# Optimization experiments

Measured on AMD Instinct MI355X. Metric: run time of the kernel, lower is better.

The kernel has to match this reference:

```python
import jax, jax.numpy as jnp
import numpy as np

N_GENE, N_DRUG = 20000, 3000
D_GENE, D_DRUG = 1024, 512
H = [256, 128]
E_GG, E_DD, E_DT = 600000, 120000, 150000
P_DROP = 0.2


def _dropout(x, key):
    # F.dropout(p=0.2, training=True) with a fixed key for determinism
    keep = jax.random.bernoulli(key, 1.0 - P_DROP, x.shape)
    return jnp.where(keep, x / (1.0 - P_DROP), 0.0).astype(x.dtype)


def _gcn_norm(x, W, b, edge_index, n):
    src, dst = edge_index[0], edge_index[1]
    loops = jnp.arange(n, dtype=src.dtype)
    src = jnp.concatenate([src, loops])
    dst = jnp.concatenate([dst, loops])
    deg = jax.ops.segment_sum(jnp.ones(src.shape, x.dtype), dst, num_segments=n)
    dinv = jax.lax.rsqrt(deg)  # deg >= 1 thanks to self loops
    xw = x @ W  # [n_src, out]
    msg = xw[src] * (dinv[src] * dinv[dst])[:, None]  # [E+n, out]
    return jax.ops.segment_sum(msg, dst, num_segments=n) + b


def _gcn_plain(x, W, b, edge_index, n_dst):
    # PyG GCNConv(add_self_loops=False, normalize=False): A X W + b (bipartite scatter)
    xw = x @ W
    return jax.ops.segment_sum(xw[edge_index[0]], edge_index[1], num_segments=n_dst) + b


def _l2norm(x):
    # F.normalize(dim=1, p=2), eps=1e-12
    n = jnp.linalg.norm(x, axis=1, keepdims=True)
    return x / jnp.maximum(n, 1e-12)


def setup_inputs() -> dict:
    key = jax.random.key(0)
    ks = jax.random.split(key, 32)
    inp = {}
    inp["gene_feat"] = jax.random.normal(ks[0], (N_GENE, D_GENE), jnp.float32)
    inp["drug_feat"] = jax.random.normal(ks[1], (N_DRUG, D_DRUG), jnp.float32)
    inp["ei_gg"] = jax.random.randint(ks[2], (2, E_GG), 0, N_GENE)
    inp["ei_dd"] = jax.random.randint(ks[3], (2, E_DD), 0, N_DRUG)
    # drug_target: messages from drug (src row) to gene (dst row)
    inp["ei_dt"] = jnp.stack([jax.random.randint(ks[4], (E_DT,), 0, N_DRUG),
                               jax.random.randint(ks[5], (E_DT,), 0, N_GENE)])
    # target_drug: messages from gene (src row) to drug (dst row)
    inp["ei_td"] = jnp.stack([jax.random.randint(ks[6], (E_DT,), 0, N_GENE),
                               jax.random.randint(ks[7], (E_DT,), 0, N_DRUG)])
    dims_in = {"gg": D_GENE, "dd": D_DRUG, "dt": D_DRUG, "td": D_GENE}
    i = 8
    for l, h in enumerate(H):
        for et in ["gg", "dd", "dt", "td"]:
            din = dims_in[et] if l == 0 else H[l - 1]
            s = float(1.0 / np.sqrt(din))
            inp[f"W{l}_{et}"] = jax.random.uniform(ks[i], (din, h), jnp.float32, -s, s)
            i += 1
            inp[f"b{l}_{et}"] = jnp.zeros((h,), jnp.float32)
    return inp


def reference(gene_feat, drug_feat, ei_gg, ei_dd, ei_dt, ei_td,
              W0_gg, b0_gg, W0_dd, b0_dd, W0_dt, b0_dt, W0_td, b0_td,
              W1_gg, b1_gg, W1_dd, b1_dd, W1_dt, b1_dt, W1_td, b1_td):
    dk = jax.random.split(jax.random.key(42), 8)
    layers = [
        ((W0_gg, b0_gg), (W0_dd, b0_dd), (W0_dt, b0_dt), (W0_td, b0_td)),
        ((W1_gg, b1_gg), (W1_dd, b1_dd), (W1_dt, b1_dt), (W1_td, b1_td)),
    ]
    xg, xd = gene_feat, drug_feat
    k = 0
    for (Wgg, bgg), (Wdd, bdd), (Wdt, bdt), (Wtd, btd) in layers:
        gg = jax.nn.relu(_gcn_norm(_dropout(xg, dk[k + 0]), Wgg, bgg, ei_gg, N_GENE))
        dd = jax.nn.relu(_gcn_norm(_dropout(xd, dk[k + 1]), Wdd, bdd, ei_dd, N_DRUG))
        dt = jax.nn.relu(_gcn_plain(_dropout(xd, dk[k + 2]), Wdt, bdt, ei_dt, N_GENE))
        td = jax.nn.relu(_gcn_plain(_dropout(xg, dk[k + 3]), Wtd, btd, ei_td, N_DRUG))
        # per-edge-type L2 normalize, then sum contributions per node type
        xg = _l2norm(gg) + _l2norm(dt)
        xd = _l2norm(dd) + _l2norm(td)
        k += 4
    # concat node-type outputs: genes first, drugs second -> [N_GENE+N_DRUG, H[-1]]
    return jnp.concatenate([xg, xd], axis=0)
```

## Files before the change

kernel.cpp:

```cpp
#include <hip/hip_runtime.h>
#include <stdint.h>

#define N_GENE 20000
#define N_DRUG 3000
#define D_GENE 1024
#define D_DRUG 512
#define H0 256
#define H1 128
#define E_GG 600000
#define E_DD 120000
#define E_DT 150000

typedef __attribute__((ext_vector_type(8))) short bf16x8;
typedef __attribute__((ext_vector_type(4))) float f32x4;

__host__ __device__ inline uint32_t rotl32(uint32_t x, int d) {
#ifdef __HIP_DEVICE_COMPILE__
    return __builtin_amdgcn_alignbit(x, x, 32 - d);
#else
    return (x << d) | (x >> (32 - d));
#endif
}

__host__ __device__ inline void tf2x32(uint32_t k0, uint32_t k1, uint32_t x0, uint32_t x1,
                                       uint32_t& o0, uint32_t& o1) {
    uint32_t ks2 = k0 ^ k1 ^ 0x1BD11BDAu;
    x0 += k0; x1 += k1;
#define TFR(r) { x0 += x1; x1 = rotl32(x1, r); x1 ^= x0; }
    TFR(13) TFR(15) TFR(26) TFR(6)
    x0 += k1; x1 += ks2 + 1u;
    TFR(17) TFR(29) TFR(16) TFR(24)
    x0 += ks2; x1 += k0 + 2u;
    TFR(13) TFR(15) TFR(26) TFR(6)
    x0 += k0; x1 += k1 + 3u;
    TFR(17) TFR(29) TFR(16) TFR(24)
    x0 += k1; x1 += ks2 + 4u;
    TFR(13) TFR(15) TFR(26) TFR(6)
    x0 += ks2; x1 += k0 + 5u;
#undef TFR
    o0 = x0; o1 = x1;
}

__device__ inline float bf_lo(uint32_t u) { return __uint_as_float(u << 16); }
__device__ inline float bf_hi(uint32_t u) { return __uint_as_float(u & 0xFFFF0000u); }

__device__ inline uint32_t drnd(float x, unsigned idx, uint32_t k0, uint32_t k1) {
    uint32_t a, b;
    tf2x32(k0, k1, 0u, idx, a, b);
    uint32_t bits = a ^ b;
    uint32_t u = __float_as_uint(x);
    uint32_t r = ((u + 0x7FFFu + ((u >> 16) & 1u)) >> 16) & 0xFFFFu;
    return ((bits >> 9) < 6710887u) ? r : 0u;
}

__device__ inline short f2bf(float f) {
    uint32_t u = __float_as_uint(f);
    uint32_t r = (u + 0x7FFFu + ((u >> 16) & 1u)) >> 16;
    return (short)r;
}

#define CUM_E0 600000u
#define CUM_E1 720000u
#define CUM_E2 870000u
#define CUM_E3 1020000u

struct Cast4P {
    unsigned c0, c1, c2, c3;
    uint32_t k0a, k1a, k0b, k1b, k0c, k1c, k0d, k1d;
};
__global__ __launch_bounds__(256) void cast4_kernel(const float* __restrict__ Xg,
                                                    const float* __restrict__ Xd,
                                                    short* __restrict__ Am, Cast4P P) {
    unsigned j = (blockIdx.x * 256u + threadIdx.x) * 8u;
    if (j >= P.c3) return;
    unsigned base; uint32_t k0, k1; const float* X;
    if (j >= P.c2)      { base = P.c2; k0 = P.k0d; k1 = P.k1d; X = Xd; }
    else if (j >= P.c1) { base = P.c1; k0 = P.k0c; k1 = P.k1c; X = Xd; }
    else if (j >= P.c0) { base = P.c0; k0 = P.k0b; k1 = P.k1b; X = Xg; }
    else                { base = 0u;   k0 = P.k0a; k1 = P.k1a; X = Xg; }
    unsigned local = j - base;
    float4 xa = *(const float4*)(X + local);
    float4 xb = *(const float4*)(X + local + 4);
    uint32_t w0 = drnd(xa.x, local + 0u, k0, k1) | (drnd(xa.y, local + 1u, k0, k1) << 16);
    uint32_t w1 = drnd(xa.z, local + 2u, k0, k1) | (drnd(xa.w, local + 3u, k0, k1) << 16);
    uint32_t w2 = drnd(xb.x, local + 4u, k0, k1) | (drnd(xb.y, local + 5u, k0, k1) << 16);
    uint32_t w3 = drnd(xb.z, local + 6u, k0, k1) | (drnd(xb.w, local + 7u, k0, k1) << 16);
    *(uint4*)(Am + j) = make_uint4(w0, w1, w2, w3);
}

__global__ void count4_kernel(const int* __restrict__ gg, const int* __restrict__ dd,
                              const int* __restrict__ dt, const int* __restrict__ td,
                              int* __restrict__ cnt) {
    unsigned e = blockIdx.x * 256u + threadIdx.x;
    if (e >= CUM_E3) return;
    const int* dsts; unsigned base, noff;
    if (e >= CUM_E2)      { dsts = td + E_DT; base = CUM_E2; noff = 43000; }
    else if (e >= CUM_E1) { dsts = dt + E_DT; base = CUM_E1; noff = 23000; }
    else if (e >= CUM_E0) { dsts = dd + E_DD; base = CUM_E0; noff = 20000; }
    else                  { dsts = gg + E_GG; base = 0;      noff = 0; }
    atomicAdd(&cnt[noff + dsts[e - base]], 1);
}

__global__ __launch_bounds__(1024) void scan_p1(const int* __restrict__ cnt,
                                                int* __restrict__ tmp, int* __restrict__ bsum) {
    __shared__ int buf[1024];
    int tid = threadIdx.x;
    int i = blockIdx.x * 1024 + tid;
    int v = (i < 46000) ? cnt[i] : 0;
    buf[tid] = v;
    __syncthreads();
    for (int off = 1; off < 1024; off <<= 1) {
        int t = (tid >= off) ? buf[tid - off] : 0;
        __syncthreads();
        buf[tid] += t;
        __syncthreads();
    }
    if (i < 46000) tmp[i] = buf[tid];
    if (tid == 1023) bsum[blockIdx.x] = buf[1023];
}

__global__ void scan_p2(int* __restrict__ bsum) {
    int lane = threadIdx.x;
    int v = (lane < 45) ? bsum[lane] : 0;
    int orig = v;
    for (int off = 1; off < 64; off <<= 1) {
        int t = __shfl_up(v, off, 64);
        if (lane >= off) v += t;
    }
    if (lane < 45) bsum[lane] = v - orig;
}

__global__ __launch_bounds__(1024) void scan_p3(const int* __restrict__ cnt,
                                                const int* __restrict__ tmp,
                                                const int* __restrict__ bsum,
                                                int* __restrict__ rpall, int* __restrict__ pos,
                                                float* __restrict__ dinv_g,
                                                float* __restrict__ dinv_d) {
    int i = blockIdx.x * 1024 + threadIdx.x;
    if (i < 46000) {
        int g = tmp[i] - cnt[i] + bsum[blockIdx.x];
        rpall[i] = g;
        pos[i] = g;
        if (i < 20000) dinv_g[i] = 1.0f / sqrtf((float)cnt[i] + 1.0f);
        else if (i < 23000) dinv_d[i - 20000] = 1.0f / sqrtf((float)cnt[i] + 1.0f);
    }
    if (i == 0) rpall[46000] = (int)CUM_E3;
}

struct CastT4P {
    unsigned c0, c1, c2, c3;
    int lgK0, lgK1, lgK2, lgK3;
    int N;
};
__device__ inline void castT_body(unsigned idx, const float* W0, const float* W1,
                                  const float* W2, const float* W3,
                                  short* __restrict__ Wt, const CastT4P& P) {
    if (idx >= P.c3) return;
    unsigned base; const float* W; int lgK;
    if (idx >= P.c2)      { base = P.c2; W = W3; lgK = P.lgK3; }
    else if (idx >= P.c1) { base = P.c1; W = W2; lgK = P.lgK2; }
    else if (idx >= P.c0) { base = P.c0; W = W1; lgK = P.lgK1; }
    else                  { base = 0u;   W = W0; lgK = P.lgK0; }
    unsigned local = idx - base;
    unsigned n = local >> lgK, k = local & ((1u << lgK) - 1u);
    Wt[idx] = f2bf(W[(size_t)k * P.N + n]);
}

__global__ __launch_bounds__(256) void fillcastT_kernel(
    const int* __restrict__ gg, const int* __restrict__ dd,
    const int* __restrict__ dt, const int* __restrict__ td,
    int* __restrict__ pos, int* __restrict__ col,
    const float* __restrict__ W0, const float* __restrict__ W1,
    const float* __restrict__ W2, const float* __restrict__ W3,
    short* __restrict__ Wt, CastT4P P, int fillBlocks) {
    int bx = blockIdx.x;
    if (bx < fillBlocks) {
        unsigned e = (unsigned)bx * 256u + threadIdx.x;
        if (e >= CUM_E3) return;
        const int* ei; unsigned base, noff; int E;
        if (e >= CUM_E2)      { ei = td; base = CUM_E2; noff = 43000; E = E_DT; }
        else if (e >= CUM_E1) { ei = dt; base = CUM_E1; noff = 23000; E = E_DT; }
        else if (e >= CUM_E0) { ei = dd; base = CUM_E0; noff = 20000; E = E_DD; }
        else                  { ei = gg; base = 0;      noff = 0;     E = E_GG; }
        unsigned local = e - base;
        int src = ei[local], dst = ei[E + local];
        int p = atomicAdd(&pos[noff + dst], 1);
        col[p] = src;
        return;
    }
    castT_body((unsigned)(bx - fillBlocks) * 256u + threadIdx.x, W0, W1, W2, W3, Wt, P);
}

struct GDesc { unsigned aoff, boff, coff; const float* rs; int M, K, mb0; };
#define LDP 72
__global__ __launch_bounds__(256) void gemm4_kernel(
    const short* __restrict__ Ab, const short* __restrict__ Wb, short* __restrict__ Cb,
    GDesc d0, GDesc d1, GDesc d2, GDesc d3, int N) {
    __shared__ short As[64 * LDP];
    __shared__ short Bs[64 * LDP];
    GDesc d;
    int bx = blockIdx.x;
    if (bx >= d3.mb0) d = d3;
    else if (bx >= d2.mb0) d = d2;
    else if (bx >= d1.mb0) d = d1;
    else d = d0;
    bx -= d.mb0;
    const short* A = Ab + d.aoff;
    const short* Bt = Wb + d.boff;
    short* C = Cb + d.coff;
    const int M = d.M, K = d.K;

    int tid = threadIdx.x;
    int lane = tid & 63;
    int w = tid >> 6;
    int m = lane & 15, kb = lane >> 4;
    int m0w = (w >> 1) * 32, n0w = (w & 1) * 32;
    int gm = bx * 64, gn = blockIdx.y * 64;

    int flat0 = tid, flat1 = tid + 256;
    int ar0 = flat0 >> 3, ac0 = (flat0 & 7) * 8;
    int ar1 = flat1 >> 3, ac1 = (flat1 & 7) * 8;
    int agr0 = min(gm + ar0, M - 1), agr1 = min(gm + ar1, M - 1);
    const short* pa0 = A + (size_t)agr0 * K + ac0;
    const short* pa1 = A + (size_t)agr1 * K + ac1;
    const short* pb0 = Bt + (size_t)(gn + ar0) * K + ac0;
    const short* pb1 = Bt + (size_t)(gn + ar1) * K + ac1;

    f32x4 acc[2][2];
#pragma unroll
    for (int i = 0; i < 2; i++)
#pragma unroll
        for (int j = 0; j < 2; j++) acc[i][j] = (f32x4){0.f, 0.f, 0.f, 0.f};

    uint4 ra0 = *(const uint4*)pa0;
    uint4 ra1 = *(const uint4*)pa1;
    uint4 rb0 = *(const uint4*)pb0;
    uint4 rb1 = *(const uint4*)pb1;

    int nt = K >> 6;
    for (int t = 0; t < nt; ++t) {
        __syncthreads();
        *(uint4*)&As[ar0 * LDP + ac0] = ra0;
        *(uint4*)&As[ar1 * LDP + ac1] = ra1;
        *(uint4*)&Bs[ar0 * LDP + ac0] = rb0;
        *(uint4*)&Bs[ar1 * LDP + ac1] = rb1;
        __syncthreads();
        if (t + 1 < nt) {
            int kt = (t + 1) << 6;
            ra0 = *(const uint4*)(pa0 + kt);
            ra1 = *(const uint4*)(pa1 + kt);
            rb0 = *(const uint4*)(pb0 + kt);
            rb1 = *(const uint4*)(pb1 + kt);
        }
#pragma unroll
        for (int ks = 0; ks < 2; ++ks) {
            bf16x8 a0 = *(const bf16x8*)&As[(m0w + m) * LDP + ks * 32 + kb * 8];
            bf16x8 a1 = *(const bf16x8*)&As[(m0w + 16 + m) * LDP + ks * 32 + kb * 8];
            bf16x8 b0 = *(const bf16x8*)&Bs[(n0w + m) * LDP + ks * 32 + kb * 8];
            bf16x8 b1 = *(const bf16x8*)&Bs[(n0w + 16 + m) * LDP + ks * 32 + kb * 8];
            acc[0][0] = __builtin_amdgcn_mfma_f32_16x16x32_bf16(a0, b0, acc[0][0], 0, 0, 0);
            acc[0][1] = __builtin_amdgcn_mfma_f32_16x16x32_bf16(a0, b1, acc[0][1], 0, 0, 0);
            acc[1][0] = __builtin_amdgcn_mfma_f32_16x16x32_bf16(a1, b0, acc[1][0], 0, 0, 0);
            acc[1][1] = __builtin_amdgcn_mfma_f32_16x16x32_bf16(a1, b1, acc[1][1], 0, 0, 0);
        }
    }
#pragma unroll
    for (int mf = 0; mf < 2; ++mf)
#pragma unroll
        for (int j = 0; j < 4; ++j) {
            int r = gm + m0w + mf * 16 + kb * 4 + j;
            if (r < M) {
                float s = (d.rs ? d.rs[r] : 1.0f) * 1.25f;
#pragma unroll
                for (int nf = 0; nf < 2; ++nf)
                    C[(size_t)r * N + gn + n0w + nf * 16 + m] = f2bf(acc[mf][nf][j] * s);
            }
        }
}

struct AggP {
    const short* XWa; const int* rpa; const float* dinv; const float* ba;
    const short* XWb; const int* rpb; const float* bb;
    float* out; int n_dst;
};

template <int F>
__device__ inline void agg_body(const AggP& P, const int* __restrict__ col, int row, int lane) {
    const int h = 64 * F;
    int c0 = lane * F;
    float acc[F], va[F];

#pragma unroll
    for (int i = 0; i < F; i++) acc[i] = 0.f;
    {
        if constexpr (F == 4) {
            uint2 u = *(const uint2*)(P.XWa + (size_t)row * h + c0);
            acc[0] += bf_lo(u.x); acc[1] += bf_hi(u.x);
            acc[2] += bf_lo(u.y); acc[3] += bf_hi(u.y);
        } else {
            uint32_t u = *(const uint32_t*)(P.XWa + (size_t)row * h + c0);
            acc[0] += bf_lo(u); acc[1] += bf_hi(u);
        }
        int s0 = P.rpa[row], s1 = P.rpa[row + 1];
        int p = s0;
        for (; p + 8 <= s1; p += 8) {
            int c[8];
#pragma unroll
            for (int i = 0; i < 8; i++) c[i] = col[p + i];
            if constexpr (F == 4) {
                uint2 g[8];
#pragma unroll
                for (int i = 0; i < 8; i++) g[i] = *(const uint2*)(P.XWa + (size_t)c[i] * h + c0);
#pragma unroll
                for (int i = 0; i < 8; i++) {
                    acc[0] += bf_lo(g[i].x); acc[1] += bf_hi(g[i].x);
                    acc[2] += bf_lo(g[i].y); acc[3] += bf_hi(g[i].y);
                }
            } else {
                uint32_t g[8];
#pragma unroll
                for (int i = 0; i < 8; i++) g[i] = *(const uint32_t*)(P.XWa + (size_t)c[i] * h + c0);
#pragma unroll
                for (int i = 0; i < 8; i++) { acc[0] += bf_lo(g[i]); acc[1] += bf_hi(g[i]); }
            }
        }
        for (; p < s1; p++) {
            int s = col[p];
            if constexpr (F == 4) {
                uint2 u = *(const uint2*)(P.XWa + (size_t)s * h + c0);
                acc[0] += bf_lo(u.x); acc[1] += bf_hi(u.x);
                acc[2] += bf_lo(u.y); acc[3] += bf_hi(u.y);
            } else {
                uint32_t u = *(const uint32_t*)(P.XWa + (size_t)s * h + c0);
                acc[0] += bf_lo(u); acc[1] += bf_hi(u);
            }
        }
    }
    float mul = P.dinv[row];
    float ssa = 0.f;
#pragma unroll
    for (int i = 0; i < F; i++) {
        float v = fmaxf(acc[i] * mul + P.ba[c0 + i], 0.f);
        va[i] = v;
        ssa += v * v;
    }

#pragma unroll
    for (int i = 0; i < F; i++) acc[i] = 0.f;
    {
        int s0 = P.rpb[row], s1 = P.rpb[row + 1];
        int p = s0;
        for (; p + 8 <= s1; p += 8) {
            int c[8];
#pragma unroll
            for (int i = 0; i < 8; i++) c[i] = col[p + i];
            if constexpr (F == 4) {
                uint2 g[8];
#pragma unroll
                for (int i = 0; i < 8; i++) g[i] = *(const uint2*)(P.XWb + (size_t)c[i] * h + c0);
#pragma unroll
                for (int i = 0; i < 8; i++) {
                    acc[0] += bf_lo(g[i].x); acc[1] += bf_hi(g[i].x);
                    acc[2] += bf_lo(g[i].y); acc[3] += bf_hi(g[i].y);
                }
            } else {
                uint32_t g[8];
#pragma unroll
                for (int i = 0; i < 8; i++) g[i] = *(const uint32_t*)(P.XWb + (size_t)c[i] * h + c0);
#pragma unroll
                for (int i = 0; i < 8; i++) { acc[0] += bf_lo(g[i]); acc[1] += bf_hi(g[i]); }
            }
        }
        for (; p < s1; p++) {
            int s = col[p];
            if constexpr (F == 4) {
                uint2 u = *(const uint2*)(P.XWb + (size_t)s * h + c0);
                acc[0] += bf_lo(u.x); acc[1] += bf_hi(u.x);
                acc[2] += bf_lo(u.y); acc[3] += bf_hi(u.y);
            } else {
                uint32_t u = *(const uint32_t*)(P.XWb + (size_t)s * h + c0);
                acc[0] += bf_lo(u); acc[1] += bf_hi(u);
            }
        }
    }
    float ssb = 0.f;
#pragma unroll
    for (int i = 0; i < F; i++) {
        float v = fmaxf(acc[i] + P.bb[c0 + i], 0.f);
        acc[i] = v;
        ssb += v * v;
    }

#pragma unroll
    for (int off = 32; off >= 1; off >>= 1) {
        ssa += __shfl_xor(ssa, off, 64);
        ssb += __shfl_xor(ssb, off, 64);
    }
    float sa = 1.0f / fmaxf(sqrtf(ssa), 1e-12f);
    float sb = 1.0f / fmaxf(sqrtf(ssb), 1e-12f);
    float* orow = P.out + (size_t)row * h + c0;
    if constexpr (F == 4) {
        *(float4*)orow = make_float4(va[0] * sa + acc[0] * sb, va[1] * sa + acc[1] * sb,
                                     va[2] * sa + acc[2] * sb, va[3] * sa + acc[3] * sb);
    } else {
        *(float2*)orow = make_float2(va[0] * sa + acc[0] * sb, va[1] * sa + acc[1] * sb);
    }
}

template <int F, bool TAIL>
__global__ __launch_bounds__(256) void agg2x_kernel(
    AggP pg, AggP pd, const int* __restrict__ col, int geneBlocks, int aggBlocks,
    const float* W0, const float* W1, const float* W2, const float* W3,
    short* Wt, CastT4P tp) {
    int bx = blockIdx.x;
    if (TAIL && bx >= aggBlocks) {
        castT_body((unsigned)(bx - aggBlocks) * 256u + threadIdx.x, W0, W1, W2, W3, Wt, tp);
        return;
    }
    int lane = threadIdx.x & 63;
    if (bx < geneBlocks) {
        int row = bx * 4 + (threadIdx.x >> 6);
        if (row < pg.n_dst) agg_body<F>(pg, col, row, lane);
    } else {
        int row = (bx - geneBlocks) * 4 + (threadIdx.x >> 6);
        if (row < pd.n_dst) agg_body<F>(pd, col, row, lane);
    }
}

extern "C" void kernel_launch(void* const* d_in, const int* in_sizes, int n_in,
                              void* d_out, int out_size, void* d_ws, size_t ws_size,
                              hipStream_t stream) {
    const float* gene = (const float*)d_in[0];
    const float* drug = (const float*)d_in[1];
    const int* ei_gg = (const int*)d_in[2];
    const int* ei_dd = (const int*)d_in[3];
    const int* ei_dt = (const int*)d_in[4];
    const int* ei_td = (const int*)d_in[5];
    const float* W0gg = (const float*)d_in[6];  const float* b0gg = (const float*)d_in[7];
    const float* W0dd = (const float*)d_in[8];  const float* b0dd = (const float*)d_in[9];
    const float* W0dt = (const float*)d_in[10]; const float* b0dt = (const float*)d_in[11];
    const float* W0td = (const float*)d_in[12]; const float* b0td = (const float*)d_in[13];
    const float* W1gg = (const float*)d_in[14]; const float* b1gg = (const float*)d_in[15];
    const float* W1dd = (const float*)d_in[16]; const float* b1dd = (const float*)d_in[17];
    const float* W1dt = (const float*)d_in[18]; const float* b1dt = (const float*)d_in[19];
    const float* W1td = (const float*)d_in[20]; const float* b1td = (const float*)d_in[21];

    uint32_t dk[8][2];
    for (uint32_t i = 0; i < 8; i++) tf2x32(0u, 42u, 0u, i, dk[i][0], dk[i][1]);

    char* p = (char*)d_ws;
    auto take = [&](size_t bytes) -> void* {
        void* r = (void*)p;
        p += (bytes + 255) & ~(size_t)255;
        return r;
    };
    short* Am   = (short*)take(sizeof(short) * 44032000ULL);
    short* XW   = (short*)take(sizeof(short) * 11776000ULL);
    short* Wt0  = (short*)take(sizeof(short) * 786432ULL);
    short* Wt1  = (short*)take(sizeof(short) * 131072ULL);
    float* xg1  = (float*)take(sizeof(float) * (size_t)N_GENE * H0);
    float* xd1  = (float*)take(sizeof(float) * (size_t)N_DRUG * H0);
    float* dinv_g = (float*)take(sizeof(float) * N_GENE);
    float* dinv_d = (float*)take(sizeof(float) * N_DRUG);
    int* cnt   = (int*)take(4 * 46000);
    int* tmp   = (int*)take(4 * 46000);
    int* bsum  = (int*)take(4 * 64);
    int* pos   = (int*)take(4 * 46000);
    int* rpall = (int*)take(4 * 46001);
    int* col   = (int*)take(4 * 1020000);

    const int* rp_gg = rpall;
    const int* rp_dd = rpall + 20000;
    const int* rp_dt = rpall + 23000;
    const int* rp_td = rpall + 43000;

    hipMemsetAsync(cnt, 0, 4 * 46000, stream);
    count4_kernel<<<(1020000 + 255) / 256, 256, 0, stream>>>(ei_gg, ei_dd, ei_dt, ei_td, cnt);

    {
        Cast4P cp = {20480000u, 40960000u, 42496000u, 44032000u,
                     dk[0][0], dk[0][1], dk[3][0], dk[3][1],
                     dk[1][0], dk[1][1], dk[2][0], dk[2][1]};
        cast4_kernel<<<(44032000 / 8 + 255) / 256, 256, 0, stream>>>(gene, drug, Am, cp);
        scan_p1<<<45, 1024, 0, stream>>>(cnt, tmp, bsum);
        scan_p2<<<1, 64, 0, stream>>>(bsum);
        scan_p3<<<45, 1024, 0, stream>>>(cnt, tmp, bsum, rpall, pos, dinv_g, dinv_d);
        CastT4P tp0 = {262144u, 524288u, 655360u, 786432u, 10, 10, 9, 9, H0};
        int fillBlocks = (1020000 + 255) / 256;
        fillcastT_kernel<<<fillBlocks + (786432 + 255) / 256, 256, 0, stream>>>(
            ei_gg, ei_dd, ei_dt, ei_td, pos, col,
            W0gg, W0td, W0dd, W0dt, Wt0, tp0, fillBlocks);

        GDesc g0 = {0u,        0u,      0u,        dinv_g,  N_GENE, 1024, 0};
        GDesc g1 = {20480000u, 262144u, 5120000u,  nullptr, N_GENE, 1024, 313};
        GDesc g2 = {40960000u, 524288u, 10240000u, dinv_d,  N_DRUG, 512,  626};
        GDesc g3 = {42496000u, 655360u, 11008000u, nullptr, N_DRUG, 512,  673};
        gemm4_kernel<<<dim3(720, H0 / 64), 256, 0, stream>>>(Am, Wt0, XW, g0, g1, g2, g3, H0);

        AggP pg = {XW, rp_gg, dinv_g, b0gg, XW + 11008000, rp_dt, b0dt, xg1, N_GENE};
        AggP pd = {XW + 10240000, rp_dd, dinv_d, b0dd, XW + 5120000, rp_td, b0td, xd1, N_DRUG};
        CastT4P tp1 = {32768u, 65536u, 98304u, 131072u, 8, 8, 8, 8, H1};
        int geneBlocks = (N_GENE + 3) / 4, aggBlocks = geneBlocks + (N_DRUG + 3) / 4;
        agg2x_kernel<4, true><<<aggBlocks + (131072 + 255) / 256, 256, 0, stream>>>(
            pg, pd, col, geneBlocks, aggBlocks, W1gg, W1td, W1dd, W1dt, Wt1, tp1);
    }

    {
        Cast4P cp = {5120000u, 10240000u, 11008000u, 11776000u,
                     dk[4][0], dk[4][1], dk[7][0], dk[7][1],
                     dk[5][0], dk[5][1], dk[6][0], dk[6][1]};
        cast4_kernel<<<(11776000 / 8 + 255) / 256, 256, 0, stream>>>(xg1, xd1, Am, cp);
        GDesc g0 = {0u,        0u,     0u,        dinv_g,  N_GENE, 256, 0};
        GDesc g1 = {5120000u,  32768u, 5120000u,  nullptr, N_GENE, 256, 313};
        GDesc g2 = {10240000u, 65536u, 10240000u, dinv_d,  N_DRUG, 256, 626};
        GDesc g3 = {11008000u, 98304u, 11008000u, nullptr, N_DRUG, 256, 673};
        gemm4_kernel<<<dim3(720, H1 / 64), 256, 0, stream>>>(Am, Wt1, XW, g0, g1, g2, g3, H1);

        float* og = (float*)d_out;
        float* od = og + (size_t)N_GENE * H1;
        AggP pg = {XW, rp_gg, dinv_g, b1gg, XW + 11008000, rp_dt, b1dt, og, N_GENE};
        AggP pd = {XW + 10240000, rp_dd, dinv_d, b1dd, XW + 5120000, rp_td, b1td, od, N_DRUG};
        CastT4P tpDummy = {0u, 0u, 0u, 0u, 0, 0, 0, 0, 0};
        int geneBlocks = (N_GENE + 3) / 4, aggBlocks = geneBlocks + (N_DRUG + 3) / 4;
        agg2x_kernel<2, false><<<aggBlocks, 256, 0, stream>>>(
            pg, pd, col, geneBlocks, aggBlocks,
            nullptr, nullptr, nullptr, nullptr, nullptr, tpDummy);
    }
}
```

Measured before the change: 410.3 us.

## Fuse dropout and bf16 cast into GEMM A-tile loads, drop staging buffer

Removes the separate cast4 pass that wrote dropped-out bf16 copies of the activations to a large staging buffer. The GEMM now reads fp32 activations directly, runs the threefry dropout mask and bf16 rounding while building each A tile, and stores it to shared memory. The GEMM tile changes to 32 rows by the full output width, so each block reads its A rows once, and launch bounds ask for 2 blocks per CU. The weight transpose-cast moves into the edge-count kernel, and the CSR fill becomes its own kernel. Costs: the RNG work sits inside the GEMM main loop, and the old register prefetch of the next tile is gone, so loads are no longer overlapped with MFMA.

New measurement: 403.2 us. Within noise of the previous version (-1.7%).

```diff
diff --git a/kernel.cpp b/kernel.cpp
--- a/kernel.cpp
+++ b/kernel.cpp
@@ -44,13 +44,14 @@
 __device__ inline float bf_lo(uint32_t u) { return __uint_as_float(u << 16); }
 __device__ inline float bf_hi(uint32_t u) { return __uint_as_float(u & 0xFFFF0000u); }
 
-__device__ inline uint32_t drnd(float x, unsigned idx, uint32_t k0, uint32_t k1) {
+__device__ inline bool tf_keep(unsigned idx, uint32_t k0, uint32_t k1) {
     uint32_t a, b;
     tf2x32(k0, k1, 0u, idx, a, b);
-    uint32_t bits = a ^ b;
+    return (((a ^ b) >> 9) < 6710887u);
+}
+__device__ inline uint32_t bfbits(float x) {
     uint32_t u = __float_as_uint(x);
-    uint32_t r = ((u + 0x7FFFu + ((u >> 16) & 1u)) >> 16) & 0xFFFFu;
-    return ((bits >> 9) < 6710887u) ? r : 0u;
+    return ((u + 0x7FFFu + ((u >> 16) & 1u)) >> 16) & 0xFFFFu;
 }
 
 __device__ inline short f2bf(float f) {
@@ -63,89 +64,6 @@
 #define CUM_E1 720000u
 #define CUM_E2 870000u
 #define CUM_E3 1020000u
-
-struct Cast4P {
-    unsigned c0, c1, c2, c3;
-    uint32_t k0a, k1a, k0b, k1b, k0c, k1c, k0d, k1d;
-};
-__global__ __launch_bounds__(256) void cast4_kernel(const float* __restrict__ Xg,
-                                                    const float* __restrict__ Xd,
-                                                    short* __restrict__ Am, Cast4P P) {
-    unsigned j = (blockIdx.x * 256u + threadIdx.x) * 8u;
-    if (j >= P.c3) return;
-    unsigned base; uint32_t k0, k1; const float* X;
-    if (j >= P.c2)      { base = P.c2; k0 = P.k0d; k1 = P.k1d; X = Xd; }
-    else if (j >= P.c1) { base = P.c1; k0 = P.k0c; k1 = P.k1c; X = Xd; }
-    else if (j >= P.c0) { base = P.c0; k0 = P.k0b; k1 = P.k1b; X = Xg; }
-    else                { base = 0u;   k0 = P.k0a; k1 = P.k1a; X = Xg; }
-    unsigned local = j - base;
-    float4 xa = *(const float4*)(X + local);
-    float4 xb = *(const float4*)(X + local + 4);
-    uint32_t w0 = drnd(xa.x, local + 0u, k0, k1) | (drnd(xa.y, local + 1u, k0, k1) << 16);
-    uint32_t w1 = drnd(xa.z, local + 2u, k0, k1) | (drnd(xa.w, local + 3u, k0, k1) << 16);
-    uint32_t w2 = drnd(xb.x, local + 4u, k0, k1) | (drnd(xb.y, local + 5u, k0, k1) << 16);
-    uint32_t w3 = drnd(xb.z, local + 6u, k0, k1) | (drnd(xb.w, local + 7u, k0, k1) << 16);
-    *(uint4*)(Am + j) = make_uint4(w0, w1, w2, w3);
-}
-
-__global__ void count4_kernel(const int* __restrict__ gg, const int* __restrict__ dd,
-                              const int* __restrict__ dt, const int* __restrict__ td,
-                              int* __restrict__ cnt) {
-    unsigned e = blockIdx.x * 256u + threadIdx.x;
-    if (e >= CUM_E3) return;
-    const int* dsts; unsigned base, noff;
-    if (e >= CUM_E2)      { dsts = td + E_DT; base = CUM_E2; noff = 43000; }
-    else if (e >= CUM_E1) { dsts = dt + E_DT; base = CUM_E1; noff = 23000; }
-    else if (e >= CUM_E0) { dsts = dd + E_DD; base = CUM_E0; noff = 20000; }
-    else                  { dsts = gg + E_GG; base = 0;      noff = 0; }
-    atomicAdd(&cnt[noff + dsts[e - base]], 1);
-}
-
-__global__ __launch_bounds__(1024) void scan_p1(const int* __restrict__ cnt,
-                                                int* __restrict__ tmp, int* __restrict__ bsum) {
-    __shared__ int buf[1024];
-    int tid = threadIdx.x;
-    int i = blockIdx.x * 1024 + tid;
-    int v = (i < 46000) ? cnt[i] : 0;
-    buf[tid] = v;
-    __syncthreads();
-    for (int off = 1; off < 1024; off <<= 1) {
-        int t = (tid >= off) ? buf[tid - off] : 0;
-        __syncthreads();
-        buf[tid] += t;
-        __syncthreads();
-    }
-    if (i < 46000) tmp[i] = buf[tid];
-    if (tid == 1023) bsum[blockIdx.x] = buf[1023];
-}
-
-__global__ void scan_p2(int* __restrict__ bsum) {
-    int lane = threadIdx.x;
-    int v = (lane < 45) ? bsum[lane] : 0;
-    int orig = v;
-    for (int off = 1; off < 64; off <<= 1) {
-        int t = __shfl_up(v, off, 64);
-        if (lane >= off) v += t;
-    }
-    if (lane < 45) bsum[lane] = v - orig;
-}
-
-__global__ __launch_bounds__(1024) void scan_p3(const int* __restrict__ cnt,
-                                                const int* __restrict__ tmp,
-                                                const int* __restrict__ bsum,
-                                                int* __restrict__ rpall, int* __restrict__ pos,
-                                                float* __restrict__ dinv_g,
-                                                float* __restrict__ dinv_d) {
-    int i = blockIdx.x * 1024 + threadIdx.x;
-    if (i < 46000) {
-        int g = tmp[i] - cnt[i] + bsum[blockIdx.x];
-        rpall[i] = g;
-        pos[i] = g;
-        if (i < 20000) dinv_g[i] = 1.0f / sqrtf((float)cnt[i] + 1.0f);
-        else if (i < 23000) dinv_d[i - 20000] = 1.0f / sqrtf((float)cnt[i] + 1.0f);
-    }
-    if (i == 0) rpall[46000] = (int)CUM_E3;
-}
 
 struct CastT4P {
     unsigned c0, c1, c2, c3;
@@ -166,114 +84,193 @@
     Wt[idx] = f2bf(W[(size_t)k * P.N + n]);
 }
 
-__global__ __launch_bounds__(256) void fillcastT_kernel(
+__global__ __launch_bounds__(256) void count4x_kernel(
+    const int* __restrict__ gg, const int* __restrict__ dd,
+    const int* __restrict__ dt, const int* __restrict__ td, int* __restrict__ cnt,
+    const float* __restrict__ W0, const float* __restrict__ W1,
+    const float* __restrict__ W2, const float* __restrict__ W3,
+    short* __restrict__ Wt, CastT4P P, int countBlocks) {
+    int bx = blockIdx.x;
+    if (bx >= countBlocks) {
+        castT_body((unsigned)(bx - countBlocks) * 256u + threadIdx.x, W0, W1, W2, W3, Wt, P);
+        return;
+    }
+    unsigned e = (unsigned)bx * 256u + threadIdx.x;
+    if (e >= CUM_E3) return;
+    const int* dsts; unsigned base, noff;
+    if (e >= CUM_E2)      { dsts = td + E_DT; base = CUM_E2; noff = 43000; }
+    else if (e >= CUM_E1) { dsts = dt + E_DT; base = CUM_E1; noff = 23000; }
+    else if (e >= CUM_E0) { dsts = dd + E_DD; base = CUM_E0; noff = 20000; }
+    else                  { dsts = gg + E_GG; base = 0;      noff = 0; }
+    atomicAdd(&cnt[noff + dsts[e - base]], 1);
+}
+
+__global__ __launch_bounds__(1024) void scan_p1(const int* __restrict__ cnt,
+                                                int* __restrict__ tmp, int* __restrict__ bsum) {
+    __shared__ int buf[1024];
+    int tid = threadIdx.x;
+    int i = blockIdx.x * 1024 + tid;
+    int v = (i < 46000) ? cnt[i] : 0;
+    buf[tid] = v;
+    __syncthreads();
+    for (int off = 1; off < 1024; off <<= 1) {
+        int t = (tid >= off) ? buf[tid - off] : 0;
+        __syncthreads();
+        buf[tid] += t;
+        __syncthreads();
+    }
+    if (i < 46000) tmp[i] = buf[tid];
+    if (tid == 1023) bsum[blockIdx.x] = buf[1023];
+}
+
+__global__ void scan_p2(int* __restrict__ bsum) {
+    int lane = threadIdx.x;
+    int v = (lane < 45) ? bsum[lane] : 0;
+    int orig = v;
+    for (int off = 1; off < 64; off <<= 1) {
+        int t = __shfl_up(v, off, 64);
+        if (lane >= off) v += t;
+    }
+    if (lane < 45) bsum[lane] = v - orig;
+}
+
+__global__ __launch_bounds__(1024) void scan_p3(const int* __restrict__ cnt,
+                                                const int* __restrict__ tmp,
+                                                const int* __restrict__ bsum,
+                                                int* __restrict__ rpall, int* __restrict__ pos,
+                                                float* __restrict__ dinv_g,
+                                                float* __restrict__ dinv_d) {
+    int i = blockIdx.x * 1024 + threadIdx.x;
+    if (i < 46000) {
+        int g = tmp[i] - cnt[i] + bsum[blockIdx.x];
+        rpall[i] = g;
+        pos[i] = g;
+        if (i < 20000) dinv_g[i] = 1.0f / sqrtf((float)cnt[i] + 1.0f);
+        else if (i < 23000) dinv_d[i - 20000] = 1.0f / sqrtf((float)cnt[i] + 1.0f);
+    }
+    if (i == 0) rpall[46000] = (int)CUM_E3;
+}
+
+__global__ __launch_bounds__(256) void fill_kernel(
     const int* __restrict__ gg, const int* __restrict__ dd,
     const int* __restrict__ dt, const int* __restrict__ td,
-    int* __restrict__ pos, int* __restrict__ col,
-    const float* __restrict__ W0, const float* __restrict__ W1,
-    const float* __restrict__ W2, const float* __restrict__ W3,
-    short* __restrict__ Wt, CastT4P P, int fillBlocks) {
-    int bx = blockIdx.x;
-    if (bx < fillBlocks) {
-        unsigned e = (unsigned)bx * 256u + threadIdx.x;
-        if (e >= CUM_E3) return;
-        const int* ei; unsigned base, noff; int E;
-        if (e >= CUM_E2)      { ei = td; base = CUM_E2; noff = 43000; E = E_DT; }
-        else if (e >= CUM_E1) { ei = dt; base = CUM_E1; noff = 23000; E = E_DT; }
-        else if (e >= CUM_E0) { ei = dd; base = CUM_E0; noff = 20000; E = E_DD; }
-        else                  { ei = gg; base = 0;      noff = 0;     E = E_GG; }
-        unsigned local = e - base;
-        int src = ei[local], dst = ei[E + local];
-        int p = atomicAdd(&pos[noff + dst], 1);
-        col[p] = src;
-        return;
-    }
-    castT_body((unsigned)(bx - fillBlocks) * 256u + threadIdx.x, W0, W1, W2, W3, Wt, P);
-}
-
-struct GDesc { unsigned aoff, boff, coff; const float* rs; int M, K, mb0; };
+    int* __restrict__ pos, int* __restrict__ col) {
+    unsigned e = blockIdx.x * 256u + threadIdx.x;
+    if (e >= CUM_E3) return;
+    const int* ei; unsigned base, noff; int E;
+    if (e >= CUM_E2)      { ei = td; base = CUM_E2; noff = 43000; E = E_DT; }
+    else if (e >= CUM_E1) { ei = dt; base = CUM_E1; noff = 23000; E = E_DT; }
+    else if (e >= CUM_E0) { ei = dd; base = CUM_E0; noff = 20000; E = E_DD; }
+    else                  { ei = gg; base = 0;      noff = 0;     E = E_GG; }
+    unsigned local = e - base;
+    int src = ei[local], dst = ei[E + local];
+    int p = atomicAdd(&pos[noff + dst], 1);
+    col[p] = src;
+}
+
+struct GDescF { const float* X; unsigned boff, coff; const float* rs; int M, K, mb0; uint32_t k0, k1; };
 #define LDP 72
-__global__ __launch_bounds__(256) void gemm4_kernel(
-    const short* __restrict__ Ab, const short* __restrict__ Wb, short* __restrict__ Cb,
-    GDesc d0, GDesc d1, GDesc d2, GDesc d3, int N) {
-    __shared__ short As[64 * LDP];
-    __shared__ short Bs[64 * LDP];
-    GDesc d;
+template <int BN>
+__global__ __launch_bounds__(256, 2) void gemmf_kernel(
+    const short* __restrict__ Wb, short* __restrict__ Cb,
+    GDescF d0, GDescF d1, GDescF d2, GDescF d3) {
+    constexpr int WN = BN / 4;
+    constexpr int NF = WN / 16;
+    constexpr int SB = BN / 32;
+    __shared__ short As[32 * LDP];
+    __shared__ short Bs[BN * LDP];
+    GDescF d;
     int bx = blockIdx.x;
     if (bx >= d3.mb0) d = d3;
     else if (bx >= d2.mb0) d = d2;
     else if (bx >= d1.mb0) d = d1;
     else d = d0;
     bx -= d.mb0;
-    const short* A = Ab + d.aoff;
+    const int M = d.M, K = d.K;
     const short* Bt = Wb + d.boff;
     short* C = Cb + d.coff;
-    const int M = d.M, K = d.K;
+    const uint32_t k0 = d.k0, k1 = d.k1;
 
     int tid = threadIdx.x;
-    int lane = tid & 63;
-    int w = tid >> 6;
+    int lane = tid & 63, w = tid >> 6;
     int m = lane & 15, kb = lane >> 4;
-    int m0w = (w >> 1) * 32, n0w = (w & 1) * 32;
-    int gm = bx * 64, gn = blockIdx.y * 64;
-
-    int flat0 = tid, flat1 = tid + 256;
-    int ar0 = flat0 >> 3, ac0 = (flat0 & 7) * 8;
-    int ar1 = flat1 >> 3, ac1 = (flat1 & 7) * 8;
-    int agr0 = min(gm + ar0, M - 1), agr1 = min(gm + ar1, M - 1);
-    const short* pa0 = A + (size_t)agr0 * K + ac0;
-    const short* pa1 = A + (size_t)agr1 * K + ac1;
-    const short* pb0 = Bt + (size_t)(gn + ar0) * K + ac0;
-    const short* pb1 = Bt + (size_t)(gn + ar1) * K + ac1;
-
-    f32x4 acc[2][2];
+    int n0w = w * WN;
+    int gm = bx * 32;
+
+    int ar = tid >> 3, ac = (tid & 7) * 8;
+    int agr = min(gm + ar, M - 1);
+    const float* pax = d.X + (size_t)agr * K + ac;
+    unsigned abase = (unsigned)agr * (unsigned)K + (unsigned)ac;
+    const short* pb = Bt + (size_t)ar * K + ac;
+    const size_t bstep = (size_t)32 * K;
+    int aslot = ar * LDP + ac;
+
+    f32x4 acc[2][NF];
 #pragma unroll
     for (int i = 0; i < 2; i++)
 #pragma unroll
-        for (int j = 0; j < 2; j++) acc[i][j] = (f32x4){0.f, 0.f, 0.f, 0.f};
-
-    uint4 ra0 = *(const uint4*)pa0;
-    uint4 ra1 = *(const uint4*)pa1;
-    uint4 rb0 = *(const uint4*)pb0;
-    uint4 rb1 = *(const uint4*)pb1;
+        for (int j = 0; j < NF; j++) acc[i][j] = (f32x4){0.f, 0.f, 0.f, 0.f};
 
     int nt = K >> 6;
     for (int t = 0; t < nt; ++t) {
+        int kt = t << 6;
+        float4 xa = *(const float4*)(pax + kt);
+        float4 xb = *(const float4*)(pax + kt + 4);
+        uint4 b0 = *(const uint4*)(pb + kt);
+        uint4 b1 = *(const uint4*)(pb + kt + bstep);
+        uint4 b2 = *(const uint4*)(pb + kt + 2 * bstep);
+        uint4 b3 = *(const uint4*)(pb + kt + 3 * bstep);
+        uint4 b4, b5, b6, b7;
+        if constexpr (SB == 8) {
+            b4 = *(const uint4*)(pb + kt + 4 * bstep);
+            b5 = *(const uint4*)(pb + kt + 5 * bstep);
+            b6 = *(const uint4*)(pb + kt + 6 * bstep);
+            b7 = *(const uint4*)(pb + kt + 7 * bstep);
+        }
+        unsigned li = abase + (unsigned)kt;
+        bool e0 = tf_keep(li + 0u, k0, k1), e1 = tf_keep(li + 1u, k0, k1);
+        bool e2 = tf_keep(li + 2u, k0, k1), e3 = tf_keep(li + 3u, k0, k1);
+        bool e4 = tf_keep(li + 4u, k0, k1), e5 = tf_keep(li + 5u, k0, k1);
+        bool e6 = tf_keep(li + 6u, k0, k1), e7 = tf_keep(li + 7u, k0, k1);
+        uint32_t w0 = (e0 ? bfbits(xa.x) : 0u) | ((e1 ? bfbits(xa.y) : 0u) << 16);
+        uint32_t w1 = (e2 ? bfbits(xa.z) : 0u) | ((e3 ? bfbits(xa.w) : 0u) << 16);
+        uint32_t w2 = (e4 ? bfbits(xb.x) : 0u) | ((e5 ? bfbits(xb.y) : 0u) << 16);
+        uint32_t w3 = (e6 ? bfbits(xb.z) : 0u) | ((e7 ? bfbits(xb.w) : 0u) << 16);
         __syncthreads();
-        *(uint4*)&As[ar0 * LDP + ac0] = ra0;
-        *(uint4*)&As[ar1 * LDP + ac1] = ra1;
-        *(uint4*)&Bs[ar0 * LDP + ac0] = rb0;
-        *(uint4*)&Bs[ar1 * LDP + ac1] = rb1;
+        *(uint4*)&As[aslot] = make_uint4(w0, w1, w2, w3);
+        *(uint4*)&Bs[aslot] = b0;
+        *(uint4*)&Bs[aslot + 32 * LDP] = b1;
+        *(uint4*)&Bs[aslot + 64 * LDP] = b2;
+        *(uint4*)&Bs[aslot + 96 * LDP] = b3;
+        if constexpr (SB == 8) {
+            *(uint4*)&Bs[aslot + 128 * LDP] = b4;
+            *(uint4*)&Bs[aslot + 160 * LDP] = b5;
+            *(uint4*)&Bs[aslot + 192 * LDP] = b6;
+            *(uint4*)&Bs[aslot + 224 * LDP] = b7;
+        }
         __syncthreads();
-        if (t + 1 < nt) {
-            int kt = (t + 1) << 6;
-            ra0 = *(const uint4*)(pa0 + kt);
-            ra1 = *(const uint4*)(pa1 + kt);
-            rb0 = *(const uint4*)(pb0 + kt);
-            rb1 = *(const uint4*)(pb1 + kt);
-        }
 #pragma unroll
         for (int ks = 0; ks < 2; ++ks) {
-            bf16x8 a0 = *(const bf16x8*)&As[(m0w + m) * LDP + ks * 32 + kb * 8];
-            bf16x8 a1 = *(const bf16x8*)&As[(m0w + 16 + m) * LDP + ks * 32 + kb * 8];
-            bf16x8 b0 = *(const bf16x8*)&Bs[(n0w + m) * LDP + ks * 32 + kb * 8];
-            bf16x8 b1 = *(const bf16x8*)&Bs[(n0w + 16 + m) * LDP + ks * 32 + kb * 8];
-            acc[0][0] = __builtin_amdgcn_mfma_f32_16x16x32_bf16(a0, b0, acc[0][0], 0, 0, 0);
-            acc[0][1] = __builtin_amdgcn_mfma_f32_16x16x32_bf16(a0, b1, acc[0][1], 0, 0, 0);
-            acc[1][0] = __builtin_amdgcn_mfma_f32_16x16x32_bf16(a1, b0, acc[1][0], 0, 0, 0);
-            acc[1][1] = __builtin_amdgcn_mfma_f32_16x16x32_bf16(a1, b1, acc[1][1], 0, 0, 0);
+            bf16x8 a0 = *(const bf16x8*)&As[m * LDP + ks * 32 + kb * 8];
+            bf16x8 a1 = *(const bf16x8*)&As[(16 + m) * LDP + ks * 32 + kb * 8];
+#pragma unroll
+            for (int nf = 0; nf < NF; nf++) {
+                bf16x8 bf = *(const bf16x8*)&Bs[(n0w + nf * 16 + m) * LDP + ks * 32 + kb * 8];
+                acc[0][nf] = __builtin_amdgcn_mfma_f32_16x16x32_bf16(a0, bf, acc[0][nf], 0, 0, 0);
+                acc[1][nf] = __builtin_amdgcn_mfma_f32_16x16x32_bf16(a1, bf, acc[1][nf], 0, 0, 0);
+            }
         }
     }
 #pragma unroll
     for (int mf = 0; mf < 2; ++mf)
 #pragma unroll
         for (int j = 0; j < 4; ++j) {
-            int r = gm + m0w + mf * 16 + kb * 4 + j;
+            int r = gm + mf * 16 + kb * 4 + j;
             if (r < M) {
                 float s = (d.rs ? d.rs[r] : 1.0f) * 1.25f;
 #pragma unroll
-                for (int nf = 0; nf < 2; ++nf)
-                    C[(size_t)r * N + gn + n0w + nf * 16 + m] = f2bf(acc[mf][nf][j] * s);
+                for (int nf = 0; nf < NF; ++nf)
+                    C[(size_t)r * BN + n0w + nf * 16 + m] = f2bf(acc[mf][nf][j] * s);
             }
         }
 }
@@ -454,7 +451,6 @@
         p += (bytes + 255) & ~(size_t)255;
         return r;
     };
-    short* Am   = (short*)take(sizeof(short) * 44032000ULL);
     short* XW   = (short*)take(sizeof(short) * 11776000ULL);
     short* Wt0  = (short*)take(sizeof(short) * 786432ULL);
     short* Wt1  = (short*)take(sizeof(short) * 131072ULL);
@@ -475,27 +471,21 @@
     const int* rp_td = rpall + 43000;
 
     hipMemsetAsync(cnt, 0, 4 * 46000, stream);
-    count4_kernel<<<(1020000 + 255) / 256, 256, 0, stream>>>(ei_gg, ei_dd, ei_dt, ei_td, cnt);
+    CastT4P tp0 = {262144u, 524288u, 655360u, 786432u, 10, 10, 9, 9, H0};
+    int countBlocks = (1020000 + 255) / 256;
+    count4x_kernel<<<countBlocks + (786432 + 255) / 256, 256, 0, stream>>>(
+        ei_gg, ei_dd, ei_dt, ei_td, cnt, W0gg, W0td, W0dd, W0dt, Wt0, tp0, countBlocks);
+    scan_p1<<<45, 1024, 0, stream>>>(cnt, tmp, bsum);
+    scan_p2<<<1, 64, 0, stream>>>(bsum);
+    scan_p3<<<45, 1024, 0, stream>>>(cnt, tmp, bsum, rpall, pos, dinv_g, dinv_d);
+    fill_kernel<<<(1020000 + 255) / 256, 256, 0, stream>>>(ei_gg, ei_dd, ei_dt, ei_td, pos, col);
 
     {
-        Cast4P cp = {20480000u, 40960000u, 42496000u, 44032000u,
-                     dk[0][0], dk[0][1], dk[3][0], dk[3][1],
-                     dk[1][0], dk[1][1], dk[2][0], dk[2][1]};
-        cast4_kernel<<<(44032000 / 8 + 255) / 256, 256, 0, stream>>>(gene, drug, Am, cp);
-        scan_p1<<<45, 1024, 0, stream>>>(cnt, tmp, bsum);
-        scan_p2<<<1, 64, 0, stream>>>(bsum);
-        scan_p3<<<45, 1024, 0, stream>>>(cnt, tmp, bsum, rpall, pos, dinv_g, dinv_d);
-        CastT4P tp0 = {262144u, 524288u, 655360u, 786432u, 10, 10, 9, 9, H0};
-        int fillBlocks = (1020000 + 255) / 256;
-        fillcastT_kernel<<<fillBlocks + (786432 + 255) / 256, 256, 0, stream>>>(
-            ei_gg, ei_dd, ei_dt, ei_td, pos, col,
-            W0gg, W0td, W0dd, W0dt, Wt0, tp0, fillBlocks);
-
-        GDesc g0 = {0u,        0u,      0u,        dinv_g,  N_GENE, 1024, 0};
-        GDesc g1 = {20480000u, 262144u, 5120000u,  nullptr, N_GENE, 1024, 313};
-        GDesc g2 = {40960000u, 524288u, 10240000u, dinv_d,  N_DRUG, 512,  626};
-        GDesc g3 = {42496000u, 655360u, 11008000u, nullptr, N_DRUG, 512,  673};
-        gemm4_kernel<<<dim3(720, H0 / 64), 256, 0, stream>>>(Am, Wt0, XW, g0, g1, g2, g3, H0);
+        GDescF g0 = {gene, 0u,      0u,        dinv_g,  N_GENE, 1024, 0,    dk[0][0], dk[0][1]};
+        GDescF g1 = {gene, 262144u, 5120000u,  nullptr, N_GENE, 1024, 625,  dk[3][0], dk[3][1]};
+        GDescF g2 = {drug, 524288u, 10240000u, dinv_d,  N_DRUG, 512,  1250, dk[1][0], dk[1][1]};
+        GDescF g3 = {drug, 655360u, 11008000u, nullptr, N_DRUG, 512,  1344, dk[2][0], dk[2][1]};
+        gemmf_kernel<256><<<1438, 256, 0, stream>>>(Wt0, XW, g0, g1, g2, g3);
 
         AggP pg = {XW, rp_gg, dinv_g, b0gg, XW + 11008000, rp_dt, b0dt, xg1, N_GENE};
         AggP pd = {XW + 10240000, rp_dd, dinv_d, b0dd, XW + 5120000, rp_td, b0td, xd1, N_DRUG};
@@ -506,15 +496,11 @@
     }
 
     {
-        Cast4P cp = {5120000u, 10240000u, 11008000u, 11776000u,
-                     dk[4][0], dk[4][1], dk[7][0], dk[7][1],
-                     dk[5][0], dk[5][1], dk[6][0], dk[6][1]};
-        cast4_kernel<<<(11776000 / 8 + 255) / 256, 256, 0, stream>>>(xg1, xd1, Am, cp);
-        GDesc g0 = {0u,        0u,     0u,        dinv_g,  N_GENE, 256, 0};
-        GDesc g1 = {5120000u,  32768u, 5120000u,  nullptr, N_GENE, 256, 313};
-        GDesc g2 = {10240000u, 65536u, 10240000u, dinv_d,  N_DRUG, 256, 626};
-        GDesc g3 = {11008000u, 98304u, 11008000u, nullptr, N_DRUG, 256, 673};
-        gemm4_kernel<<<dim3(720, H1 / 64), 256, 0, stream>>>(Am, Wt1, XW, g0, g1, g2, g3, H1);
+        GDescF g0 = {xg1, 0u,     0u,        dinv_g,  N_GENE, 256, 0,    dk[4][0], dk[4][1]};
+        GDescF g1 = {xg1, 32768u, 5120000u,  nullptr, N_GENE, 256, 625,  dk[7][0], dk[7][1]};
+        GDescF g2 = {xd1, 65536u, 10240000u, dinv_d,  N_DRUG, 256, 1250, dk[5][0], dk[5][1]};
+        GDescF g3 = {xd1, 98304u, 11008000u, nullptr, N_DRUG, 256, 1344, dk[6][0], dk[6][1]};
+        gemmf_kernel<128><<<1438, 256, 0, stream>>>(Wt1, XW, g0, g1, g2, g3);
 
         float* og = (float*)d_out;
         float* od = og + (size_t)N_GENE * H1;
```
